# Kernel tuning notes

Measured on AMD Instinct MI355X. Metric: run time of the kernel, lower is better.

## Reference

```python
import jax, jax.numpy as jnp
import numpy as np
import math

NUM_HEADS = 8
Q_STRIDE = 2
KV_STRIDE = 2
POS_MAG = 1.0
WAVE_LEN = 1000.0


def _pos_embedding(h, w, h_kv, w_kv, feat_dim):
    # sinusoidal embedding of coordinate differences (in input-resolution units)
    h_idxs = jnp.arange(h, dtype=jnp.float32) * Q_STRIDE
    w_idxs = jnp.arange(w, dtype=jnp.float32) * Q_STRIDE
    h_kv_idxs = jnp.arange(h_kv, dtype=jnp.float32) * KV_STRIDE
    w_kv_idxs = jnp.arange(w_kv, dtype=jnp.float32) * KV_STRIDE
    h_diff = (h_idxs[:, None] - h_kv_idxs[None, :]) * POS_MAG  # [h, h_kv]
    w_diff = (w_idxs[:, None] - w_kv_idxs[None, :]) * POS_MAG  # [w, w_kv]
    feat_range = jnp.arange(feat_dim // 4, dtype=jnp.float32)
    dim_mat = WAVE_LEN ** (4.0 / feat_dim * feat_range)       # [feat_dim/4]
    ang_x = w_diff[:, :, None] / dim_mat                       # [w, w_kv, feat_dim/4]
    ang_y = h_diff[:, :, None] / dim_mat                       # [h, h_kv, feat_dim/4]
    emb_x = jnp.concatenate([jnp.sin(ang_x), jnp.cos(ang_x)], axis=2)  # [w, w_kv, feat_dim/2]
    emb_y = jnp.concatenate([jnp.sin(ang_y), jnp.cos(ang_y)], axis=2)  # [h, h_kv, feat_dim/2]
    return emb_x, emb_y


def setup_inputs() -> dict:
    key = jax.random.key(0)
    ks = jax.random.split(key, 10)
    n, C, H, W = 2, 256, 96, 96
    s = 0.05
    return {
        "x": jax.random.normal(ks[0], (n, C, H, W), jnp.float32),
        "Wq": jax.random.normal(ks[1], (C, C), jnp.float32) * s,
        "Wk": jax.random.normal(ks[2], (C, C), jnp.float32) * s,
        "Wv": jax.random.normal(ks[3], (C, C), jnp.float32) * s,
        "Wx": jax.random.normal(ks[4], (C, C // 2), jnp.float32) * s,
        "Wy": jax.random.normal(ks[5], (C, C // 2), jnp.float32) * s,
        "appr_bias": jax.random.normal(ks[6], (C,), jnp.float32) * s,
        "Wp": jax.random.normal(ks[7], (C, C), jnp.float32) * s,
        "bp": jax.random.normal(ks[8], (C,), jnp.float32) * s,
        "gamma": jax.random.normal(ks[9], (1,), jnp.float32),
    }


def reference(x, Wq, Wk, Wv, Wx, Wy, appr_bias, Wp, bp, gamma):
    n, C, H, W = x.shape
    g = NUM_HEADS
    d = C // g  # qk_embed_dim == v_dim
    # AvgPool2d(kernel_size=1, stride=s) == strided subsampling
    x_q = x[:, :, ::Q_STRIDE, ::Q_STRIDE]
    x_kv = x[:, :, ::KV_STRIDE, ::KV_STRIDE]
    h, w = x_q.shape[2], x_q.shape[3]
    h_kv, w_kv = x_kv.shape[2], x_kv.shape[3]

    # 1x1 convs (no bias) == channel matmuls
    q = jnp.einsum('oc,nchw->nohw', Wq, x_q)   # [n, C, h, w]
    k = jnp.einsum('oc,nchw->nohw', Wk, x_kv)  # [n, C, h_kv, w_kv]
    v = jnp.einsum('oc,nchw->nohw', Wv, x_kv)  # [n, C, h_kv, w_kv]

    emb_x, emb_y = _pos_embedding(h, w, h_kv, w_kv, C)
    inv_sqrt2 = 1.0 / math.sqrt(2.0)
    # Linear(feat_dim/2 -> C), split into heads, scale by 1/sqrt(2)
    pos_x = (jnp.einsum('wvf,of->wvo', emb_x, Wx).reshape(w, w_kv, g, d)
             .transpose(2, 0, 1, 3)) * inv_sqrt2  # [g, w, w_kv, d]
    pos_y = (jnp.einsum('huf,of->huo', emb_y, Wy).reshape(h, h_kv, g, d)
             .transpose(2, 0, 1, 3)) * inv_sqrt2  # [g, h, h_kv, d]

    qr = q.reshape(n, g, d, h, w).transpose(0, 1, 3, 4, 2)  # [n, g, h, w, d]
    kr = k.reshape(n, g, d, h_kv * w_kv)                     # [n, g, d, kv]

    # bias . key term, broadcast over query positions
    e_key = jnp.einsum('gd,ngdk->ngk', appr_bias.reshape(g, d), kr)
    e_key = e_key.reshape(n, g, 1, 1, h_kv, w_kv)
    # query . pos_x term (broadcast over h_kv), query . pos_y term (broadcast over w_kv)
    e_x = jnp.einsum('nghwd,gwvd->nghwv', qr, pos_x)[:, :, :, :, None, :]
    e_y = jnp.einsum('nghwd,ghud->nghwu', qr, pos_y)[:, :, :, :, :, None]

    energy = (e_key + e_x + e_y).reshape(n, g, h * w, h_kv * w_kv)
    attn = jax.nn.softmax(energy, axis=-1)  # [n, g, hw, kv]

    vr = v.reshape(n, g, d, h_kv * w_kv)  # [n, g, d, kv]
    out = jnp.einsum('ngqk,ngdk->ngdq', attn, vr).reshape(n, C, h, w)

    out = jnp.einsum('oc,nchw->nohw', Wp, out) + bp[None, :, None, None]
    out = jax.image.resize(out, (n, C, H, W), method='bilinear')
    return gamma * out + x
```

## Files before the change

### kernel.cpp

```cpp
#include <hip/hip_runtime.h>
#include <hip/hip_bf16.h>
#include <math.h>

#define NB 2
#define CC 256
#define NPOS 2304
#define NDELTA 95

typedef __attribute__((ext_vector_type(8))) short short8;
typedef __attribute__((ext_vector_type(4))) float floatx4;

__device__ inline unsigned short f2bf(float x) {
    unsigned int u = __float_as_uint(x);
    u = (u + 0x7FFFu + ((u >> 16) & 1u)) >> 16;
    return (unsigned short)u;
}
__device__ inline float bf2f(unsigned short h) {
    return __uint_as_float(((unsigned int)h) << 16);
}
__device__ inline unsigned int pk2(float a, float b) {
    return (unsigned int)f2bf(a) | ((unsigned int)f2bf(b) << 16);
}
__device__ inline unsigned int pkmul(unsigned int a, unsigned int b) {
    __hip_bfloat162 x = *(__hip_bfloat162*)&a;
    __hip_bfloat162 y = *(__hip_bfloat162*)&b;
    __hip_bfloat162 r = __hmul2(x, y);
    return *(unsigned int*)&r;
}

__global__ __launch_bounds__(256) void prep_kernel(
    const float* __restrict__ Wx, const float* __restrict__ Wy,
    const float* __restrict__ Wk, const float* __restrict__ ab,
    const float* __restrict__ Wq, const float* __restrict__ Wv,
    const float* __restrict__ Wp,
    unsigned short* __restrict__ posxb, unsigned short* __restrict__ posyb,
    unsigned short* __restrict__ Wb, unsigned short* __restrict__ Wpb)
{
    int b = blockIdx.x;
    int t = threadIdx.x;
    if (b < NDELTA) {
        __shared__ float emb[128];
        float delta = (float)(b - 47);
        if (t < 64) {
            float dim_inv = exp2f(-(float)t * 0.15571537944784511f);
            float ang = 2.0f * delta * dim_inv;
            emb[t]      = sinf(ang);
            emb[t + 64] = cosf(ang);
        }
        __syncthreads();
        float sx = 0.f, sy = 0.f;
        const float* wxr = Wx + t * 128;
        const float* wyr = Wy + t * 128;
        for (int f = 0; f < 128; ++f) {
            float e = emb[f];
            sx += e * wxr[f];
            sy += e * wyr[f];
        }
        const float inv_sqrt2 = 0.70710678118654752440f;
        int g = t >> 5, d = t & 31;
        posxb[((size_t)g * 96 + b) * 32 + d] = f2bf(sx * inv_sqrt2);
        posyb[((size_t)g * 96 + b) * 32 + d] = f2bf(sy * inv_sqrt2);
    } else if (b == NDELTA) {
        int g = t >> 5, d = t & 31;
        posxb[((size_t)g * 96 + 95) * 32 + d] = 0;
        posyb[((size_t)g * 96 + 95) * 32 + d] = 0;
    } else if (b < 96 + 640) {
        int o = b - 96;
        float v = 0.f;
        if (o < 256)      v = Wq[o * 256 + t];
        else if (o < 512) v = Wv[(o - 256) * 256 + t];
        else if (o < 520) {
            int g = o - 512;
            float s = 0.f;
            for (int d = 0; d < 32; ++d)
                s += ab[g * 32 + d] * Wk[(g * 32 + d) * 256 + t];
            v = s;
        }
        Wb[(size_t)o * 256 + t] = f2bf(v);
    } else {
        int o = b - 736;
        Wpb[(size_t)o * 256 + t] = f2bf(Wp[o * 256 + t]);
    }
}

__global__ __launch_bounds__(256) void extract_kernel(
    const float* __restrict__ x, unsigned short* __restrict__ xs_t)
{
    __shared__ __align__(16) unsigned short Lt[64][264];
    int blk = blockIdx.x;
    int pt = blk % 36;
    int n = blk / 36;
    int p0 = pt * 64;
    int t = threadIdx.x;
    int cw = t >> 4;
    int pl = t & 15;

    for (int cc = 0; cc < 16; ++cc) {
        int c = cc * 16 + cw;
        const float* src = x + ((size_t)(n * 256 + c)) * (96 * 96);
        #pragma unroll
        for (int k = 0; k < 4; ++k) {
            int p = p0 + pl + k * 16;
            int i = p / 48, j = p - i * 48;
            Lt[pl + k * 16][c] = f2bf(src[(2 * i) * 96 + 2 * j]);
        }
    }
    __syncthreads();
    #pragma unroll
    for (int it = 0; it < 8; ++it) {
        int s = t + it * 256;
        int p = s >> 5, c8 = s & 31;
        uint4 v = *(const uint4*)&Lt[p][c8 * 8];
        *(uint4*)(xs_t + ((size_t)(n * NPOS + p0 + p)) * 256 + c8 * 8) = v;
    }
}

__global__ __launch_bounds__(256, 2) void qkv_kernel(
    const unsigned short* __restrict__ xs_t, const unsigned short* __restrict__ Wb,
    unsigned short* __restrict__ qbuf, float* __restrict__ vbuf,
    float* __restrict__ ek)
{
    int mT = blockIdx.x;
    int nT = blockIdx.y;
    int t = threadIdx.x;
    int wm = t >> 6, L = t & 63, l16 = L & 15, oct = L >> 4;
    int colBase = nT * 64;
    int n = colBase / NPOS;
    int p0 = colBase - n * NPOS;
    int o_w = mT * 128 + wm * 32;

    const unsigned short* A0 = Wb + (size_t)(o_w + l16) * 256 + oct * 8;
    const unsigned short* A1 = A0 + 16 * 256;
    const unsigned short* B0 = xs_t + ((size_t)(n * NPOS + p0 + l16)) * 256 + oct * 8;

    floatx4 acc[2][4] = {};
    #pragma unroll
    for (int kc = 0; kc < 8; ++kc) {
        int k0 = kc * 32;
        short8 a0 = *(const short8*)(A0 + k0);
        short8 a1 = *(const short8*)(A1 + k0);
        short8 b0 = *(const short8*)(B0 + k0);
        short8 b1 = *(const short8*)(B0 + 16 * 256 + k0);
        short8 b2 = *(const short8*)(B0 + 32 * 256 + k0);
        short8 b3 = *(const short8*)(B0 + 48 * 256 + k0);
        acc[0][0] = __builtin_amdgcn_mfma_f32_16x16x32_bf16(a0, b0, acc[0][0], 0, 0, 0);
        acc[0][1] = __builtin_amdgcn_mfma_f32_16x16x32_bf16(a0, b1, acc[0][1], 0, 0, 0);
        acc[0][2] = __builtin_amdgcn_mfma_f32_16x16x32_bf16(a0, b2, acc[0][2], 0, 0, 0);
        acc[0][3] = __builtin_amdgcn_mfma_f32_16x16x32_bf16(a0, b3, acc[0][3], 0, 0, 0);
        acc[1][0] = __builtin_amdgcn_mfma_f32_16x16x32_bf16(a1, b0, acc[1][0], 0, 0, 0);
        acc[1][1] = __builtin_amdgcn_mfma_f32_16x16x32_bf16(a1, b1, acc[1][1], 0, 0, 0);
        acc[1][2] = __builtin_amdgcn_mfma_f32_16x16x32_bf16(a1, b2, acc[1][2], 0, 0, 0);
        acc[1][3] = __builtin_amdgcn_mfma_f32_16x16x32_bf16(a1, b3, acc[1][3], 0, 0, 0);
    }

    #pragma unroll
    for (int af = 0; af < 2; ++af) {
        #pragma unroll
        for (int f = 0; f < 4; ++f) {
            int p = p0 + f * 16 + l16;
            #pragma unroll
            for (int r = 0; r < 4; ++r) {
                int o = o_w + af * 16 + oct * 4 + r;
                float val = acc[af][f][r];
                if (o < 256) {
                    int g = o >> 5, d = o & 31;
                    qbuf[((size_t)(n * 8 + g) * NPOS + p) * 32 + d] = f2bf(val);
                } else if (o < 512) {
                    vbuf[((size_t)(n * 256 + (o - 256))) * NPOS + p] = val;
                } else if (o < 520) {
                    ek[((size_t)(n * 8 + (o - 512))) * NPOS + p] = val;
                }
            }
        }
    }
}

__global__ __launch_bounds__(256) void softA_kernel(float* __restrict__ ekA)
{
    int ng = blockIdx.x;
    float* e = ekA + (size_t)ng * NPOS;
    int t = threadIdx.x;
    __shared__ float red[256];
    float m = -1e30f;
    for (int k = t; k < NPOS; k += 256) m = fmaxf(m, e[k]);
    red[t] = m;
    __syncthreads();
    for (int s = 128; s > 0; s >>= 1) {
        if (t < s) red[t] = fmaxf(red[t], red[t + s]);
        __syncthreads();
    }
    m = red[0];
    for (int k = t; k < NPOS; k += 256) e[k] = __expf(e[k] - m);
}

__global__ __launch_bounds__(256) void vhat_kernel(
    const float* __restrict__ vbuf, const float* __restrict__ ekA,
    uint4* __restrict__ vhat)
{
    int tile = blockIdx.x;
    int ng = blockIdx.y;
    int k0 = tile * 96;
    int t = threadIdx.x;
    const float* vb = vbuf + (size_t)ng * 32 * NPOS;
    const float* Ab = ekA + (size_t)ng * NPOS;
    uint4* out = vhat + ((size_t)ng * 24 + tile) * 576;

    for (int s = t; s < 576; s += 256) {
        int grp = s >> 6;
        int Ls = s & 63;
        int cc = grp / 3;
        int nn = grp - cc * 3;
        int koct = cc * 32 + ((Ls >> 4) << 3);
        uint4 w = make_uint4(0u, 0u, 0u, 0u);
        if (nn < 2) {
            int d = nn * 16 + (Ls & 15);
            const float* vp = vb + (size_t)d * NPOS + k0 + koct;
            const float* ap = Ab + k0 + koct;
            float4 v0 = *(const float4*)vp;
            float4 v1 = *(const float4*)(vp + 4);
            float4 a0 = *(const float4*)ap;
            float4 a1 = *(const float4*)(ap + 4);
            w.x = pk2(v0.x * a0.x, v0.y * a0.y);
            w.y = pk2(v0.z * a0.z, v0.w * a0.w);
            w.z = pk2(v1.x * a1.x, v1.y * a1.y);
            w.w = pk2(v1.z * a1.z, v1.w * a1.w);
        } else if ((Ls & 15) == 0) {
            const float* ap = Ab + k0 + koct;
            float4 a0 = *(const float4*)ap;
            float4 a1 = *(const float4*)(ap + 4);
            w.x = pk2(a0.x, a0.y);
            w.y = pk2(a0.z, a0.w);
            w.z = pk2(a1.x, a1.y);
            w.w = pk2(a1.z, a1.w);
        }
        out[s] = w;
    }
}

#define DO_TILE(BB, TT) do {                                                   \
    int u0_ = (TT) * 2;                                                        \
    unsigned int y0_ = Ys[qp * 50 + u0_];     y0_ |= y0_ << 16;                \
    unsigned int y1_ = Ys[qp * 50 + u0_ + 1]; y1_ |= y1_ << 16;                \
    unsigned int Yc0_ = y0_, Yc1_ = (o < 2) ? y0_ : y1_, Yc2_ = y1_;           \
    union { unsigned int u[4]; short8 s; } av_;                                \
    av_.u[0] = pkmul(Xp[0], Yc0_); av_.u[1] = pkmul(Xp[1], Yc0_);              \
    av_.u[2] = pkmul(Xp[2], Yc0_); av_.u[3] = pkmul(Xp[3], Yc0_);              \
    acc0 = __builtin_amdgcn_mfma_f32_16x16x32_bf16(av_.s, *(const short8*)&BB[0], acc0, 0, 0, 0); \
    acc1 = __builtin_amdgcn_mfma_f32_16x16x32_bf16(av_.s, *(const short8*)&BB[1], acc1, 0, 0, 0); \
    acc2 = __builtin_amdgcn_mfma_f32_16x16x32_bf16(av_.s, *(const short8*)&BB[2], acc2, 0, 0, 0); \
    av_.u[0] = pkmul(Xp[4], Yc1_); av_.u[1] = pkmul(Xp[5], Yc1_);              \
    av_.u[2] = pkmul(Xp[6], Yc1_); av_.u[3] = pkmul(Xp[7], Yc1_);              \
    acc0 = __builtin_amdgcn_mfma_f32_16x16x32_bf16(av_.s, *(const short8*)&BB[3], acc0, 0, 0, 0); \
    acc1 = __builtin_amdgcn_mfma_f32_16x16x32_bf16(av_.s, *(const short8*)&BB[4], acc1, 0, 0, 0); \
    acc2 = __builtin_amdgcn_mfma_f32_16x16x32_bf16(av_.s, *(const short8*)&BB[5], acc2, 0, 0, 0); \
    av_.u[0] = pkmul(Xp[8], Yc2_); av_.u[1] = pkmul(Xp[9], Yc2_);              \
    av_.u[2] = pkmul(Xp[10], Yc2_); av_.u[3] = pkmul(Xp[11], Yc2_);            \
    acc0 = __builtin_amdgcn_mfma_f32_16x16x32_bf16(av_.s, *(const short8*)&BB[6], acc0, 0, 0, 0); \
    acc1 = __builtin_amdgcn_mfma_f32_16x16x32_bf16(av_.s, *(const short8*)&BB[7], acc1, 0, 0, 0); \
    acc2 = __builtin_amdgcn_mfma_f32_16x16x32_bf16(av_.s, *(const short8*)&BB[8], acc2, 0, 0, 0); \
} while (0)

__global__ __launch_bounds__(256, 2) void attn_kernel(
    const unsigned short* __restrict__ qbuf, const unsigned short* __restrict__ posxb,
    const unsigned short* __restrict__ posyb, const uint4* __restrict__ vhat,
    unsigned short* __restrict__ oattn_t)
{
    __shared__ unsigned short Xs[64 * 50];
    __shared__ unsigned short Ys[64 * 50];
    __shared__ float linv_s[64];

    int blk = blockIdx.x;
    int qt = blk % 36;
    int ng = blk / 36;
    int nb = ng >> 3, g = ng & 7;
    int qbase = qt * 64;
    int t = threadIdx.x;
    int m = t >> 6, L = t & 63;
    int l16 = L & 15, oct = L >> 4;

    {
        int qtile0 = qbase + m * 16;
        int hq = qtile0 / 48;
        int wq0 = qtile0 - hq * 48;
        short8 aq = *(const short8*)(qbuf +
            ((size_t)ng * NPOS + qtile0 + l16) * 32 + oct * 8);
        const unsigned short* pxg = posxb + (size_t)g * 96 * 32;
        const unsigned short* pyg = posyb + (size_t)g * 96 * 32;
        floatx4 zero = {0.f, 0.f, 0.f, 0.f};
        #pragma unroll
        for (int j = 0; j < 6; ++j) {
            int dl = j * 16 + l16;
            short8 bx = *(const short8*)(pxg + (size_t)dl * 32 + oct * 8);
            short8 by = *(const short8*)(pyg + (size_t)dl * 32 + oct * 8);
            floatx4 tx = __builtin_amdgcn_mfma_f32_16x16x32_bf16(aq, bx, zero, 0, 0, 0);
            floatx4 ty = __builtin_amdgcn_mfma_f32_16x16x32_bf16(aq, by, zero, 0, 0, 0);
            int u = hq + 47 - dl;
            bool uok = (u >= 0) && (u < 48);
            #pragma unroll
            for (int r = 0; r < 4; ++r) {
                int ql = oct * 4 + r;
                int v = wq0 + ql + 47 - dl;
                if (v >= 0 && v < 48)
                    Xs[(m * 16 + ql) * 50 + v] = f2bf(__expf(tx[r]));
                if (uok)
                    Ys[(m * 16 + ql) * 50 + u] = f2bf(__expf(ty[r]));
            }
        }
    }
    __syncthreads();

    int qp = m * 16 + l16;
    int o = oct;
    unsigned int Xp[12];
    #pragma unroll
    for (int c = 0; c < 3; ++c)
        #pragma unroll
        for (int jj = 0; jj < 4; ++jj) {
            int k = c * 32 + o * 8 + jj * 2;
            int v0 = (k < 48) ? k : k - 48;
            Xp[c * 4 + jj] = *(const unsigned int*)&Xs[qp * 50 + v0];
        }

    floatx4 acc0 = {0.f, 0.f, 0.f, 0.f};
    floatx4 acc1 = {0.f, 0.f, 0.f, 0.f};
    floatx4 acc2 = {0.f, 0.f, 0.f, 0.f};

    const uint4* vb = vhat + (size_t)ng * 24 * 576 + L;
    uint4 Abuf[9], Bbuf[9];
    #pragma unroll
    for (int gg = 0; gg < 9; ++gg) Abuf[gg] = vb[gg * 64];

    for (int tile = 0; tile < 24; tile += 2) {
        const uint4* sB = vb + (tile + 1) * 576;
        #pragma unroll
        for (int gg = 0; gg < 9; ++gg) Bbuf[gg] = sB[gg * 64];
        DO_TILE(Abuf, tile);
        if (tile + 2 < 24) {
            const uint4* sA = vb + (tile + 2) * 576;
            #pragma unroll
            for (int gg = 0; gg < 9; ++gg) Abuf[gg] = sA[gg * 64];
        }
        DO_TILE(Bbuf, tile + 1);
    }

    if ((L & 15) == 0) {
        int qc = m * 16 + (L >> 4) * 4;
        #pragma unroll
        for (int r = 0; r < 4; ++r)
            linv_s[qc + r] = 1.0f / acc2[r];
    }
    __syncthreads();
    {
        int qc = m * 16 + (L >> 4) * 4;
        int d0 = L & 15;
        #pragma unroll
        for (int r = 0; r < 4; ++r) {
            float lir = linv_s[qc + r];
            size_t row = ((size_t)nb * NPOS + qbase + qc + r) * 256;
            oattn_t[row + g * 32 + d0]      = f2bf(acc0[r] * lir);
            oattn_t[row + g * 32 + 16 + d0] = f2bf(acc1[r] * lir);
        }
    }
}

__global__ __launch_bounds__(256, 2) void proj_kernel(
    const unsigned short* __restrict__ oattn_t, const unsigned short* __restrict__ Wpb,
    const float* __restrict__ bpv, unsigned short* __restrict__ projb)
{
    int mT = blockIdx.x;
    int nT = blockIdx.y;
    int t = threadIdx.x;
    int wm = t >> 6, L = t & 63, l16 = L & 15, oct = L >> 4;
    int colBase = nT * 64;
    int n = colBase / NPOS;
    int p0 = colBase - n * NPOS;
    int o_w = mT * 128 + wm * 32;

    const unsigned short* A0 = Wpb + (size_t)(o_w + l16) * 256 + oct * 8;
    const unsigned short* A1 = A0 + 16 * 256;
    const unsigned short* B0 = oattn_t + ((size_t)(n * NPOS + p0 + l16)) * 256 + oct * 8;

    floatx4 acc[2][4] = {};
    #pragma unroll
    for (int kc = 0; kc < 8; ++kc) {
        int k0 = kc * 32;
        short8 a0 = *(const short8*)(A0 + k0);
        short8 a1 = *(const short8*)(A1 + k0);
        short8 b0 = *(const short8*)(B0 + k0);
        short8 b1 = *(const short8*)(B0 + 16 * 256 + k0);
        short8 b2 = *(const short8*)(B0 + 32 * 256 + k0);
        short8 b3 = *(const short8*)(B0 + 48 * 256 + k0);
        acc[0][0] = __builtin_amdgcn_mfma_f32_16x16x32_bf16(a0, b0, acc[0][0], 0, 0, 0);
        acc[0][1] = __builtin_amdgcn_mfma_f32_16x16x32_bf16(a0, b1, acc[0][1], 0, 0, 0);
        acc[0][2] = __builtin_amdgcn_mfma_f32_16x16x32_bf16(a0, b2, acc[0][2], 0, 0, 0);
        acc[0][3] = __builtin_amdgcn_mfma_f32_16x16x32_bf16(a0, b3, acc[0][3], 0, 0, 0);
        acc[1][0] = __builtin_amdgcn_mfma_f32_16x16x32_bf16(a1, b0, acc[1][0], 0, 0, 0);
        acc[1][1] = __builtin_amdgcn_mfma_f32_16x16x32_bf16(a1, b1, acc[1][1], 0, 0, 0);
        acc[1][2] = __builtin_amdgcn_mfma_f32_16x16x32_bf16(a1, b2, acc[1][2], 0, 0, 0);
        acc[1][3] = __builtin_amdgcn_mfma_f32_16x16x32_bf16(a1, b3, acc[1][3], 0, 0, 0);
    }

    #pragma unroll
    for (int af = 0; af < 2; ++af) {
        #pragma unroll
        for (int f = 0; f < 4; ++f) {
            int p = p0 + f * 16 + l16;
            #pragma unroll
            for (int r = 0; r < 4; ++r) {
                int o = o_w + af * 16 + oct * 4 + r;
                projb[((size_t)(n * 256 + o)) * NPOS + p] = f2bf(acc[af][f][r] + bpv[o]);
            }
        }
    }
}

__global__ __launch_bounds__(256) void resize_kernel(
    const unsigned short* __restrict__ projb, const float* __restrict__ x,
    const float* __restrict__ gamma, float* __restrict__ out)
{
    int idx = blockIdx.x * 256 + threadIdx.x;
    int J = idx % 96;
    int tmp = idx / 96;
    int I = tmp % 96;
    int nc = tmp / 96;

    int jr = I >> 1;
    int r0, r1; float w0, w1;
    if ((I & 1) == 0) { r0 = (jr > 0) ? jr - 1 : 0; r1 = jr; w0 = 0.25f; w1 = 0.75f; }
    else              { r0 = jr; r1 = (jr < 47) ? jr + 1 : 47; w0 = 0.75f; w1 = 0.25f; }
    int jc = J >> 1;
    int c0, c1; float u0, u1;
    if ((J & 1) == 0) { c0 = (jc > 0) ? jc - 1 : 0; c1 = jc; u0 = 0.25f; u1 = 0.75f; }
    else              { c0 = jc; c1 = (jc < 47) ? jc + 1 : 47; u0 = 0.75f; u1 = 0.25f; }

    const unsigned short* P = projb + (size_t)nc * NPOS;
    float v = w0 * (u0 * bf2f(P[r0 * 48 + c0]) + u1 * bf2f(P[r0 * 48 + c1])) +
              w1 * (u0 * bf2f(P[r1 * 48 + c0]) + u1 * bf2f(P[r1 * 48 + c1]));
    out[idx] = gamma[0] * v + x[idx];
}

extern "C" void kernel_launch(void* const* d_in, const int* in_sizes, int n_in,
                              void* d_out, int out_size, void* d_ws, size_t ws_size,
                              hipStream_t stream)
{
    const float* x     = (const float*)d_in[0];
    const float* Wq    = (const float*)d_in[1];
    const float* Wk    = (const float*)d_in[2];
    const float* Wv    = (const float*)d_in[3];
    const float* Wx    = (const float*)d_in[4];
    const float* Wy    = (const float*)d_in[5];
    const float* ab    = (const float*)d_in[6];
    const float* Wp    = (const float*)d_in[7];
    const float* bp    = (const float*)d_in[8];
    const float* gamma = (const float*)d_in[9];
    float* out = (float*)d_out;

    unsigned short* posxb = (unsigned short*)d_ws;
    unsigned short* posyb  = posxb + 8 * 96 * 32;
    unsigned short* Wb     = posyb + 8 * 96 * 32;
    unsigned short* Wpb    = Wb + (size_t)640 * 256;
    unsigned short* xs_t   = Wpb + (size_t)256 * 256;
    unsigned short* qbuf   = xs_t + (size_t)2 * NPOS * 256;
    unsigned short* oattn_t= qbuf + (size_t)2 * NPOS * 256;
    unsigned short* projb  = oattn_t + (size_t)2 * NPOS * 256;
    float* vbuf  = (float*)(projb + (size_t)2 * NPOS * 256);
    float* ekA   = vbuf + (size_t)2 * 256 * NPOS;
    uint4* vhat  = (uint4*)(ekA + 16 * NPOS);

    hipLaunchKernelGGL(prep_kernel, dim3(992), dim3(256), 0, stream,
                       Wx, Wy, Wk, ab, Wq, Wv, Wp, posxb, posyb, Wb, Wpb);
    hipLaunchKernelGGL(extract_kernel, dim3(72), dim3(256), 0, stream, x, xs_t);
    hipLaunchKernelGGL(qkv_kernel, dim3(5, 72), dim3(256), 0, stream,
                       xs_t, Wb, qbuf, vbuf, ekA);
    hipLaunchKernelGGL(softA_kernel, dim3(16), dim3(256), 0, stream, ekA);
    hipLaunchKernelGGL(vhat_kernel, dim3(24, 16), dim3(256), 0, stream,
                       vbuf, ekA, vhat);
    hipLaunchKernelGGL(attn_kernel, dim3(576), dim3(256), 0, stream,
                       qbuf, posxb, posyb, vhat, oattn_t);
    hipLaunchKernelGGL(proj_kernel, dim3(2, 72), dim3(256), 0, stream,
                       oattn_t, Wpb, bp, projb);
    hipLaunchKernelGGL(resize_kernel, dim3((2 * 256 * 96 * 96) / 256), dim3(256), 0, stream,
                       projb, x, gamma, out);
}
```

Baseline: 169.7 us.

## Merge prep and extract kernels, drop softmax max pass, vectorize stores

Folds the subsample/transpose extract kernel into the prep kernel as extra blocks, saving one launch. Removes the separate softA max-subtraction kernel and computes exp of the bias-key term directly inside vhat_kernel via shared memory, skipping the max reduction (overflow risk if the energies are large). Specializes the qkv epilogue per output region with packed bf16 q stores, and vectorizes the resize kernel to four outputs per thread with float4 loads and stores.

```diff
diff --git a/kernel.cpp b/kernel.cpp
--- a/kernel.cpp
+++ b/kernel.cpp
@@ -28,18 +28,20 @@
     return *(unsigned int*)&r;
 }
 
-__global__ __launch_bounds__(256) void prep_kernel(
+__global__ __launch_bounds__(256) void prep_extract_kernel(
     const float* __restrict__ Wx, const float* __restrict__ Wy,
     const float* __restrict__ Wk, const float* __restrict__ ab,
     const float* __restrict__ Wq, const float* __restrict__ Wv,
-    const float* __restrict__ Wp,
+    const float* __restrict__ Wp, const float* __restrict__ x,
     unsigned short* __restrict__ posxb, unsigned short* __restrict__ posyb,
-    unsigned short* __restrict__ Wb, unsigned short* __restrict__ Wpb)
-{
+    unsigned short* __restrict__ Wb, unsigned short* __restrict__ Wpb,
+    unsigned short* __restrict__ xs_t)
+{
+    __shared__ __align__(16) unsigned short Lt[64][264];
     int b = blockIdx.x;
     int t = threadIdx.x;
     if (b < NDELTA) {
-        __shared__ float emb[128];
+        float* emb = (float*)&Lt[0][0];
         float delta = (float)(b - 47);
         if (t < 64) {
             float dim_inv = exp2f(-(float)t * 0.15571537944784511f);
@@ -77,41 +79,35 @@
             v = s;
         }
         Wb[(size_t)o * 256 + t] = f2bf(v);
-    } else {
+    } else if (b < 992) {
         int o = b - 736;
         Wpb[(size_t)o * 256 + t] = f2bf(Wp[o * 256 + t]);
-    }
-}
-
-__global__ __launch_bounds__(256) void extract_kernel(
-    const float* __restrict__ x, unsigned short* __restrict__ xs_t)
-{
-    __shared__ __align__(16) unsigned short Lt[64][264];
-    int blk = blockIdx.x;
-    int pt = blk % 36;
-    int n = blk / 36;
-    int p0 = pt * 64;
-    int t = threadIdx.x;
-    int cw = t >> 4;
-    int pl = t & 15;
-
-    for (int cc = 0; cc < 16; ++cc) {
-        int c = cc * 16 + cw;
-        const float* src = x + ((size_t)(n * 256 + c)) * (96 * 96);
-        #pragma unroll
-        for (int k = 0; k < 4; ++k) {
-            int p = p0 + pl + k * 16;
-            int i = p / 48, j = p - i * 48;
-            Lt[pl + k * 16][c] = f2bf(src[(2 * i) * 96 + 2 * j]);
-        }
-    }
-    __syncthreads();
-    #pragma unroll
-    for (int it = 0; it < 8; ++it) {
-        int s = t + it * 256;
-        int p = s >> 5, c8 = s & 31;
-        uint4 v = *(const uint4*)&Lt[p][c8 * 8];
-        *(uint4*)(xs_t + ((size_t)(n * NPOS + p0 + p)) * 256 + c8 * 8) = v;
+    } else {
+        int blk = b - 992;
+        int pt = blk % 36;
+        int n = blk / 36;
+        int p0 = pt * 64;
+        int cw = t >> 4;
+        int pl = t & 15;
+
+        for (int cc = 0; cc < 16; ++cc) {
+            int c = cc * 16 + cw;
+            const float* src = x + ((size_t)(n * 256 + c)) * (96 * 96);
+            #pragma unroll
+            for (int k = 0; k < 4; ++k) {
+                int p = p0 + pl + k * 16;
+                int i = p / 48, j = p - i * 48;
+                Lt[pl + k * 16][c] = f2bf(src[(2 * i) * 96 + 2 * j]);
+            }
+        }
+        __syncthreads();
+        #pragma unroll
+        for (int it = 0; it < 8; ++it) {
+            int s = t + it * 256;
+            int p = s >> 5, c8 = s & 31;
+            uint4 v = *(const uint4*)&Lt[p][c8 * 8];
+            *(uint4*)(xs_t + ((size_t)(n * NPOS + p0 + p)) * 256 + c8 * 8) = v;
+        }
     }
 }
 
@@ -153,48 +149,52 @@
         acc[1][3] = __builtin_amdgcn_mfma_f32_16x16x32_bf16(a1, b3, acc[1][3], 0, 0, 0);
     }
 
-    #pragma unroll
-    for (int af = 0; af < 2; ++af) {
-        #pragma unroll
-        for (int f = 0; f < 4; ++f) {
-            int p = p0 + f * 16 + l16;
-            #pragma unroll
-            for (int r = 0; r < 4; ++r) {
-                int o = o_w + af * 16 + oct * 4 + r;
-                float val = acc[af][f][r];
-                if (o < 256) {
-                    int g = o >> 5, d = o & 31;
-                    qbuf[((size_t)(n * 8 + g) * NPOS + p) * 32 + d] = f2bf(val);
-                } else if (o < 512) {
-                    vbuf[((size_t)(n * 256 + (o - 256))) * NPOS + p] = val;
-                } else if (o < 520) {
-                    ek[((size_t)(n * 8 + (o - 512))) * NPOS + p] = val;
+    if (o_w < 256) {
+        #pragma unroll
+        for (int af = 0; af < 2; ++af) {
+            int ob = o_w + af * 16 + oct * 4;
+            int g = ob >> 5, d0 = ob & 31;
+            #pragma unroll
+            for (int f = 0; f < 4; ++f) {
+                int p = p0 + f * 16 + l16;
+                uint2 w;
+                w.x = pk2(acc[af][f][0], acc[af][f][1]);
+                w.y = pk2(acc[af][f][2], acc[af][f][3]);
+                *(uint2*)&qbuf[((size_t)(n * 8 + g) * NPOS + p) * 32 + d0] = w;
+            }
+        }
+    } else if (o_w < 512) {
+        #pragma unroll
+        for (int af = 0; af < 2; ++af) {
+            #pragma unroll
+            for (int f = 0; f < 4; ++f) {
+                int p = p0 + f * 16 + l16;
+                #pragma unroll
+                for (int r = 0; r < 4; ++r) {
+                    int o = o_w + af * 16 + oct * 4 + r;
+                    vbuf[((size_t)(n * 256 + (o - 256))) * NPOS + p] = acc[af][f][r];
                 }
             }
         }
-    }
-}
-
-__global__ __launch_bounds__(256) void softA_kernel(float* __restrict__ ekA)
-{
-    int ng = blockIdx.x;
-    float* e = ekA + (size_t)ng * NPOS;
-    int t = threadIdx.x;
-    __shared__ float red[256];
-    float m = -1e30f;
-    for (int k = t; k < NPOS; k += 256) m = fmaxf(m, e[k]);
-    red[t] = m;
-    __syncthreads();
-    for (int s = 128; s > 0; s >>= 1) {
-        if (t < s) red[t] = fmaxf(red[t], red[t + s]);
-        __syncthreads();
-    }
-    m = red[0];
-    for (int k = t; k < NPOS; k += 256) e[k] = __expf(e[k] - m);
+    } else {
+        #pragma unroll
+        for (int af = 0; af < 2; ++af) {
+            #pragma unroll
+            for (int f = 0; f < 4; ++f) {
+                int p = p0 + f * 16 + l16;
+                #pragma unroll
+                for (int r = 0; r < 4; ++r) {
+                    int o = o_w + af * 16 + oct * 4 + r;
+                    if (o < 520)
+                        ek[((size_t)(n * 8 + (o - 512))) * NPOS + p] = acc[af][f][r];
+                }
+            }
+        }
+    }
 }
 
 __global__ __launch_bounds__(256) void vhat_kernel(
-    const float* __restrict__ vbuf, const float* __restrict__ ekA,
+    const float* __restrict__ vbuf, const float* __restrict__ ek,
     uint4* __restrict__ vhat)
 {
     int tile = blockIdx.x;
@@ -202,8 +202,11 @@
     int k0 = tile * 96;
     int t = threadIdx.x;
     const float* vb = vbuf + (size_t)ng * 32 * NPOS;
-    const float* Ab = ekA + (size_t)ng * NPOS;
     uint4* out = vhat + ((size_t)ng * 24 + tile) * 576;
+
+    __shared__ __align__(16) float Ae[96];
+    if (t < 96) Ae[t] = __expf(ek[(size_t)ng * NPOS + k0 + t]);
+    __syncthreads();
 
     for (int s = t; s < 576; s += 256) {
         int grp = s >> 6;
@@ -215,7 +218,7 @@
         if (nn < 2) {
             int d = nn * 16 + (Ls & 15);
             const float* vp = vb + (size_t)d * NPOS + k0 + koct;
-            const float* ap = Ab + k0 + koct;
+            const float* ap = Ae + koct;
             float4 v0 = *(const float4*)vp;
             float4 v1 = *(const float4*)(vp + 4);
             float4 a0 = *(const float4*)ap;
@@ -225,7 +228,7 @@
             w.z = pk2(v1.x * a1.x, v1.y * a1.y);
             w.w = pk2(v1.z * a1.z, v1.w * a1.w);
         } else if ((Ls & 15) == 0) {
-            const float* ap = Ab + k0 + koct;
+            const float* ap = Ae + koct;
             float4 a0 = *(const float4*)ap;
             float4 a1 = *(const float4*)(ap + 4);
             w.x = pk2(a0.x, a0.y);
@@ -418,9 +421,9 @@
     const unsigned short* __restrict__ projb, const float* __restrict__ x,
     const float* __restrict__ gamma, float* __restrict__ out)
 {
-    int idx = blockIdx.x * 256 + threadIdx.x;
-    int J = idx % 96;
-    int tmp = idx / 96;
+    int idx4 = blockIdx.x * 256 + threadIdx.x;
+    int J0 = (idx4 % 24) * 4;
+    int tmp = idx4 / 24;
     int I = tmp % 96;
     int nc = tmp / 96;
 
@@ -428,15 +431,26 @@
     int r0, r1; float w0, w1;
     if ((I & 1) == 0) { r0 = (jr > 0) ? jr - 1 : 0; r1 = jr; w0 = 0.25f; w1 = 0.75f; }
     else              { r0 = jr; r1 = (jr < 47) ? jr + 1 : 47; w0 = 0.75f; w1 = 0.25f; }
-    int jc = J >> 1;
-    int c0, c1; float u0, u1;
-    if ((J & 1) == 0) { c0 = (jc > 0) ? jc - 1 : 0; c1 = jc; u0 = 0.25f; u1 = 0.75f; }
-    else              { c0 = jc; c1 = (jc < 47) ? jc + 1 : 47; u0 = 0.75f; u1 = 0.25f; }
 
     const unsigned short* P = projb + (size_t)nc * NPOS;
-    float v = w0 * (u0 * bf2f(P[r0 * 48 + c0]) + u1 * bf2f(P[r0 * 48 + c1])) +
-              w1 * (u0 * bf2f(P[r1 * 48 + c0]) + u1 * bf2f(P[r1 * 48 + c1]));
-    out[idx] = gamma[0] * v + x[idx];
+    size_t base = ((size_t)nc * 96 + I) * 96 + J0;
+    float4 xv = *(const float4*)(x + base);
+    float gm = gamma[0];
+    float4 ov;
+    #pragma unroll
+    for (int k = 0; k < 4; ++k) {
+        int J = J0 + k;
+        int jc = J >> 1;
+        int c0, c1; float u0, u1;
+        if ((J & 1) == 0) { c0 = (jc > 0) ? jc - 1 : 0; c1 = jc; u0 = 0.25f; u1 = 0.75f; }
+        else              { c0 = jc; c1 = (jc < 47) ? jc + 1 : 47; u0 = 0.75f; u1 = 0.25f; }
+        float v = w0 * (u0 * bf2f(P[r0 * 48 + c0]) + u1 * bf2f(P[r0 * 48 + c1])) +
+                  w1 * (u0 * bf2f(P[r1 * 48 + c0]) + u1 * bf2f(P[r1 * 48 + c1]));
+        float xr = (k == 0) ? xv.x : (k == 1) ? xv.y : (k == 2) ? xv.z : xv.w;
+        float o = gm * v + xr;
+        if (k == 0) ov.x = o; else if (k == 1) ov.y = o; else if (k == 2) ov.z = o; else ov.w = o;
+    }
+    *(float4*)(out + base) = ov;
 }
 
 extern "C" void kernel_launch(void* const* d_in, const int* in_sizes, int n_in,
@@ -464,21 +478,19 @@
     unsigned short* oattn_t= qbuf + (size_t)2 * NPOS * 256;
     unsigned short* projb  = oattn_t + (size_t)2 * NPOS * 256;
     float* vbuf  = (float*)(projb + (size_t)2 * NPOS * 256);
-    float* ekA   = vbuf + (size_t)2 * 256 * NPOS;
-    uint4* vhat  = (uint4*)(ekA + 16 * NPOS);
-
-    hipLaunchKernelGGL(prep_kernel, dim3(992), dim3(256), 0, stream,
-                       Wx, Wy, Wk, ab, Wq, Wv, Wp, posxb, posyb, Wb, Wpb);
-    hipLaunchKernelGGL(extract_kernel, dim3(72), dim3(256), 0, stream, x, xs_t);
+    float* ek    = vbuf + (size_t)2 * 256 * NPOS;
+    uint4* vhat  = (uint4*)(ek + 16 * NPOS);
+
+    hipLaunchKernelGGL(prep_extract_kernel, dim3(1064), dim3(256), 0, stream,
+                       Wx, Wy, Wk, ab, Wq, Wv, Wp, x, posxb, posyb, Wb, Wpb, xs_t);
     hipLaunchKernelGGL(qkv_kernel, dim3(5, 72), dim3(256), 0, stream,
-                       xs_t, Wb, qbuf, vbuf, ekA);
-    hipLaunchKernelGGL(softA_kernel, dim3(16), dim3(256), 0, stream, ekA);
+                       xs_t, Wb, qbuf, vbuf, ek);
     hipLaunchKernelGGL(vhat_kernel, dim3(24, 16), dim3(256), 0, stream,
-                       vbuf, ekA, vhat);
+                       vbuf, ek, vhat);
     hipLaunchKernelGGL(attn_kernel, dim3(576), dim3(256), 0, stream,
                        qbuf, posxb, posyb, vhat, oattn_t);
     hipLaunchKernelGGL(proj_kernel, dim3(2, 72), dim3(256), 0, stream,
                        oattn_t, Wpb, bp, projb);
-    hipLaunchKernelGGL(resize_kernel, dim3((2 * 256 * 96 * 96) / 256), dim3(256), 0, stream,
+    hipLaunchKernelGGL(resize_kernel, dim3((2 * 256 * 96 * 96) / (256 * 4)), dim3(256), 0, stream,
                        projb, x, gamma, out);
 }
```

New measurement: 152.9 us. 9.9% less time.
